# Performance work log

Hardware: AMD Instinct MI355X
Metric: run time of the kernel (lower is better)

Reference implementation:

```python
import jax, jax.numpy as jnp
import numpy as np

B, D_IN = 2048, 16
Q, QD = 512, 2
H = 128

def setup_inputs() -> dict:
    key = jax.random.key(0)
    ks = jax.random.split(key, 7)
    return {
        "input": jax.random.normal(ks[0], (B, D_IN), dtype=jnp.float32),
        "eq_param": jax.random.normal(ks[1], (QD, 1), dtype=jnp.float32),
        "quad_x": jax.random.uniform(ks[2], (Q, QD), dtype=jnp.float32),
        "W1": jax.random.normal(ks[3], (QD + D_IN, H), dtype=jnp.float32) * (1.0 / np.sqrt(QD + D_IN)),
        "b1": jnp.zeros((H,), dtype=jnp.float32),
        "W2": jax.random.normal(ks[4], (H, 1), dtype=jnp.float32) * (1.0 / np.sqrt(H)),
        "b2": jnp.zeros((1,), dtype=jnp.float32),
    }

def reference(input, eq_param, quad_x, W1, b1, W2, b2):
    # input: [B, d_in], quad_x: [Q, qd]
    b, d = input.shape
    q, qd = quad_x.shape
    # x = quad_x.repeat(B,1) -> [B,Q,qd]; z = input repeated per quad row -> [B,Q,d]
    x = jnp.broadcast_to(quad_x[None, :, :], (b, q, qd))
    z = jnp.broadcast_to(input[:, None, :], (b, q, d))
    concat = jnp.concatenate([x, z], axis=-1)            # [B,Q,qd+d]
    h = jnp.tanh(concat @ W1 + b1)                       # [B,Q,H]
    lhs = h @ W2 + b2                                    # [B,Q,1]  (mlp_x)
    y = jnp.sin(x @ eq_param)                            # [B,Q,1]  (r_func)
    rhs = lhs * y
    # per-row segment sum over Q quadrature points (and scalar out dim)
    out = jnp.sum(rhs, axis=(1, 2))[:, None]             # [B,1]
    return out
```

## Files before the change

### kernel.cpp

```cpp
#include <hip/hip_runtime.h>
#include <math.h>

#define B_N   2048
#define D_IN_ 16
#define Q_N   512
#define H_N   128

#define QCHUNK 32
#define QPC    (QCHUNK / 4)
#define NQC_A  8
#define QCHUNK_B 16
#define QPC_B    (QCHUNK_B / 4)
#define NQC_B    16

#define NB     8
#define RPB    16
#define NRB    (B_N / RPB)

static constexpr float kC = 2.88539008177792681472f;

__global__ __launch_bounds__(256, 4) void fused_kernel_a(
    const float* __restrict__ input,
    const float* __restrict__ eq,
    const float* __restrict__ qx,
    const float* __restrict__ W1,
    const float* __restrict__ b1,
    const float* __restrict__ W2,
    const float* __restrict__ b2,
    float* __restrict__ out)
{
    __shared__ float c_s[QPC * 8 * H_N];
    __shared__ float in_s[RPB * D_IN_];
    __shared__ float qx_s[QCHUNK * 2];
    __shared__ float y_s[QCHUNK];
    __shared__ float part[4][NB];
    __shared__ float Sc_s, w2sum_s;

    const int t    = threadIdx.x;
    const int rb   = blockIdx.x & (NRB - 1);
    const int qc   = blockIdx.x >> 7;
    const int h    = t & 127;
    const int bg   = t >> 7;
    const int lane = t & 63;
    const int w    = t >> 6;

    in_s[t] = input[rb * (RPB * D_IN_) + t];
    if (t < QCHUNK * 2) qx_s[t] = qx[qc * (QCHUNK * 2) + t];
    if (w == 0) {
        float s = 0.0f;
        if (lane < QCHUNK) {
            const int q = qc * QCHUNK + lane;
            const float a  = fmaf(qx[2 * q + 1], eq[1], qx[2 * q] * eq[0]);
            const float yv = sinf(a);
            y_s[lane] = -2.0f * yv;
            s = yv;
        }
        #pragma unroll
        for (int off = 32; off >= 1; off >>= 1)
            s += __shfl_down(s, off, 64);
        if (lane == 0) Sc_s = s;
    }
    if (w == 1) {
        float s = W2[lane] + W2[64 + lane];
        #pragma unroll
        for (int off = 32; off >= 1; off >>= 1)
            s += __shfl_down(s, off, 64);
        if (lane == 0) w2sum_s = s;
    }
    const float w2 = W2[h];
    __syncthreads();

    {
        const float w1a = W1[h], w1b = W1[H_N + h], bh = b1[h];
        #pragma unroll
        for (int k = 0; k < 4; ++k) {
            const int qd = bg * 4 + k;
            float n0 = 0, n1 = 0, n2 = 0, n3 = 0;
            float p1 = 0, p2 = 0, p3 = 0, p4 = 0;
            #pragma unroll
            for (int i = 0; i < 4; ++i) {
                const int ql = qd * 4 + i;
                const float x0 = qx_s[2 * ql], x1 = qx_s[2 * ql + 1];
                const float u = fmaf(x1, w1b, fmaf(x0, w1a, bh));
                const float E = __builtin_amdgcn_exp2f(u * kC);
                const float y = y_s[ql];
                n3 = fmaf(E, n2, fmaf(y, p3, n3));
                n2 = fmaf(E, n1, fmaf(y, p2, n2));
                n1 = fmaf(E, n0, fmaf(y, p1, n1));
                n0 = n0 + y;
                p4 = fmaf(E, p3, p4);
                p3 = fmaf(E, p2, p3);
                p2 = fmaf(E, p1, p2);
                p1 = p1 + E;
            }
            float* dst = c_s + qd * (8 * H_N) + h;
            dst[0 * H_N] = n0; dst[1 * H_N] = n1;
            dst[2 * H_N] = n2; dst[3 * H_N] = n3;
            dst[4 * H_N] = p1; dst[5 * H_N] = p2;
            dst[6 * H_N] = p3; dst[7 * H_N] = p4;
        }
    }

    float F[NB], acc[NB];
    {
        float s[NB];
        #pragma unroll
        for (int r = 0; r < NB; ++r) s[r] = 0.0f;
        const float4* in4 = (const float4*)in_s;
        #pragma unroll
        for (int k = 0; k < 4; ++k) {
            const float wa = W1[(2 + 4 * k + 0) * H_N + h];
            const float wb = W1[(2 + 4 * k + 1) * H_N + h];
            const float wc = W1[(2 + 4 * k + 2) * H_N + h];
            const float wd = W1[(2 + 4 * k + 3) * H_N + h];
            #pragma unroll
            for (int r = 0; r < NB; ++r) {
                const float4 a = in4[(bg * NB + r) * 4 + k];
                float sr = s[r];
                sr = fmaf(a.x, wa, sr);
                sr = fmaf(a.y, wb, sr);
                sr = fmaf(a.z, wc, sr);
                sr = fmaf(a.w, wd, sr);
                s[r] = sr;
            }
        }
        #pragma unroll
        for (int r = 0; r < NB; ++r) {
            F[r] = __builtin_amdgcn_exp2f(s[r] * kC);
            acc[r] = 0.0f;
        }
    }
    __syncthreads();

    #pragma unroll 2
    for (int qd = 0; qd < QPC; ++qd) {
        const float* cp = c_s + qd * (8 * H_N) + h;
        const float n0 = cp[0 * H_N], n1 = cp[1 * H_N];
        const float n2 = cp[2 * H_N], n3 = cp[3 * H_N];
        const float c1 = cp[4 * H_N], c2 = cp[5 * H_N];
        const float c3 = cp[6 * H_N], c4 = cp[7 * H_N];
        #pragma unroll
        for (int r = 0; r < NB; ++r) {
            const float Fr  = F[r];
            const float den = fmaf(fmaf(fmaf(fmaf(c4, Fr, c3), Fr, c2), Fr, c1), Fr, 1.0f);
            const float num = fmaf(fmaf(fmaf(n3, Fr, n2), Fr, n1), Fr, n0);
            acc[r] = fmaf(num, __builtin_amdgcn_rcpf(den), acc[r]);
        }
    }

    #pragma unroll
    for (int r = 0; r < NB; ++r) {
        float p = acc[r] * w2;
        #pragma unroll
        for (int off = 32; off >= 1; off >>= 1)
            p += __shfl_down(p, off, 64);
        if (lane == 0) part[w][r] = p;
    }
    __syncthreads();

    if (t < 16) {
        const int r = t & 7, g = t >> 3;
        const float k0c = Sc_s * (w2sum_s + b2[0]);
        const float s = part[2 * g][r] + part[2 * g + 1][r] + k0c;
        atomicAdd(out + rb * RPB + g * NB + r, s);
    }
}

__global__ __launch_bounds__(256, 8) void fused_kernel_b(
    const float* __restrict__ input,
    const float* __restrict__ eq,
    const float* __restrict__ qx,
    const float* __restrict__ W1,
    const float* __restrict__ b1,
    const float* __restrict__ W2,
    const float* __restrict__ b2,
    float* __restrict__ out)
{
    __shared__ float c_s[QPC_B * 8 * H_N];
    __shared__ float in_s[RPB * D_IN_];
    __shared__ float qx_s[QCHUNK_B * 2];
    __shared__ float y_s[QCHUNK_B];
    __shared__ float part[4][NB];
    __shared__ float Sc_s, w2sum_s;

    const int t    = threadIdx.x;
    const int rb   = blockIdx.x & (NRB - 1);
    const int qc   = 16 + (blockIdx.x >> 7);
    const int h    = t & 127;
    const int bg   = t >> 7;
    const int lane = t & 63;
    const int w    = t >> 6;

    in_s[t] = input[rb * (RPB * D_IN_) + t];
    if (t < QCHUNK_B * 2) qx_s[t] = qx[qc * (QCHUNK_B * 2) + t];
    if (w == 0) {
        float s = 0.0f;
        if (lane < QCHUNK_B) {
            const int q = qc * QCHUNK_B + lane;
            const float a  = fmaf(qx[2 * q + 1], eq[1], qx[2 * q] * eq[0]);
            const float yv = sinf(a);
            y_s[lane] = -2.0f * yv;
            s = yv;
        }
        #pragma unroll
        for (int off = 32; off >= 1; off >>= 1)
            s += __shfl_down(s, off, 64);
        if (lane == 0) Sc_s = s;
    }
    if (w == 1) {
        float s = W2[lane] + W2[64 + lane];
        #pragma unroll
        for (int off = 32; off >= 1; off >>= 1)
            s += __shfl_down(s, off, 64);
        if (lane == 0) w2sum_s = s;
    }
    const float w2 = W2[h];
    __syncthreads();

    {
        const float w1a = W1[h], w1b = W1[H_N + h], bh = b1[h];
        #pragma unroll
        for (int k = 0; k < 2; ++k) {
            const int qd = bg * 2 + k;
            float n0 = 0, n1 = 0, n2 = 0, n3 = 0;
            float p1 = 0, p2 = 0, p3 = 0, p4 = 0;
            #pragma unroll
            for (int i = 0; i < 4; ++i) {
                const int ql = qd * 4 + i;
                const float x0 = qx_s[2 * ql], x1 = qx_s[2 * ql + 1];
                const float u = fmaf(x1, w1b, fmaf(x0, w1a, bh));
                const float E = __builtin_amdgcn_exp2f(u * kC);
                const float y = y_s[ql];
                n3 = fmaf(E, n2, fmaf(y, p3, n3));
                n2 = fmaf(E, n1, fmaf(y, p2, n2));
                n1 = fmaf(E, n0, fmaf(y, p1, n1));
                n0 = n0 + y;
                p4 = fmaf(E, p3, p4);
                p3 = fmaf(E, p2, p3);
                p2 = fmaf(E, p1, p2);
                p1 = p1 + E;
            }
            float* dst = c_s + qd * (8 * H_N) + h;
            dst[0 * H_N] = n0; dst[1 * H_N] = n1;
            dst[2 * H_N] = n2; dst[3 * H_N] = n3;
            dst[4 * H_N] = p1; dst[5 * H_N] = p2;
            dst[6 * H_N] = p3; dst[7 * H_N] = p4;
        }
    }

    float F[NB], acc[NB];
    {
        float s[NB];
        #pragma unroll
        for (int r = 0; r < NB; ++r) s[r] = 0.0f;
        const float4* in4 = (const float4*)in_s;
        #pragma unroll
        for (int k = 0; k < 4; ++k) {
            const float wa = W1[(2 + 4 * k + 0) * H_N + h];
            const float wb = W1[(2 + 4 * k + 1) * H_N + h];
            const float wc = W1[(2 + 4 * k + 2) * H_N + h];
            const float wd = W1[(2 + 4 * k + 3) * H_N + h];
            #pragma unroll
            for (int r = 0; r < NB; ++r) {
                const float4 a = in4[(bg * NB + r) * 4 + k];
                float sr = s[r];
                sr = fmaf(a.x, wa, sr);
                sr = fmaf(a.y, wb, sr);
                sr = fmaf(a.z, wc, sr);
                sr = fmaf(a.w, wd, sr);
                s[r] = sr;
            }
        }
        #pragma unroll
        for (int r = 0; r < NB; ++r) {
            F[r] = __builtin_amdgcn_exp2f(s[r] * kC);
            acc[r] = 0.0f;
        }
    }
    __syncthreads();

    #pragma unroll 2
    for (int qd = 0; qd < QPC_B; ++qd) {
        const float* cp = c_s + qd * (8 * H_N) + h;
        const float n0 = cp[0 * H_N], n1 = cp[1 * H_N];
        const float n2 = cp[2 * H_N], n3 = cp[3 * H_N];
        const float c1 = cp[4 * H_N], c2 = cp[5 * H_N];
        const float c3 = cp[6 * H_N], c4 = cp[7 * H_N];
        #pragma unroll
        for (int r = 0; r < NB; ++r) {
            const float Fr  = F[r];
            const float den = fmaf(fmaf(fmaf(fmaf(c4, Fr, c3), Fr, c2), Fr, c1), Fr, 1.0f);
            const float num = fmaf(fmaf(fmaf(n3, Fr, n2), Fr, n1), Fr, n0);
            acc[r] = fmaf(num, __builtin_amdgcn_rcpf(den), acc[r]);
        }
    }

    #pragma unroll
    for (int r = 0; r < NB; ++r) {
        float p = acc[r] * w2;
        #pragma unroll
        for (int off = 32; off >= 1; off >>= 1)
            p += __shfl_down(p, off, 64);
        if (lane == 0) part[w][r] = p;
    }
    __syncthreads();

    if (t < 16) {
        const int r = t & 7, g = t >> 3;
        const float k0c = Sc_s * (w2sum_s + b2[0]);
        const float s = part[2 * g][r] + part[2 * g + 1][r] + k0c;
        atomicAdd(out + rb * RPB + g * NB + r, s);
    }
}

extern "C" void kernel_launch(void* const* d_in, const int* in_sizes, int n_in,
                              void* d_out, int out_size, void* d_ws, size_t ws_size,
                              hipStream_t stream)
{
    (void)in_sizes; (void)n_in; (void)d_ws; (void)ws_size;
    const float* input = (const float*)d_in[0];
    const float* eq    = (const float*)d_in[1];
    const float* qx    = (const float*)d_in[2];
    const float* W1    = (const float*)d_in[3];
    const float* b1    = (const float*)d_in[4];
    const float* W2    = (const float*)d_in[5];
    const float* b2    = (const float*)d_in[6];
    float* out = (float*)d_out;

    hipMemsetAsync(d_out, 0, (size_t)out_size * sizeof(float), stream);
    fused_kernel_a<<<dim3(NRB * NQC_A), dim3(256), 0, stream>>>(
        input, eq, qx, W1, b1, W2, b2, out);
    fused_kernel_b<<<dim3(NRB * NQC_B), dim3(256), 0, stream>>>(
        input, eq, qx, W1, b1, W2, b2, out);
}
```

Before: 87.16 us.

## Split into precompute kernel for F and per-chunk coefficients plus lean main kernel

Adds a precompute kernel that computes the per-row exp factors F (B×H) and the per-quadrature-chunk rational coefficients once and writes them to the workspace. A second kernel then reads them as float4s from global memory and does only the rational evaluation and reduction. This removes the 128-fold redundant coefficient computation and 16-fold redundant F computation done in every block. In exchange it adds an extra launch and about 1 MB of global traffic for F. A fallback fused kernel with swizzled float4 shared storage is kept for when no workspace is provided.

```diff
diff --git a/kernel.cpp b/kernel.cpp
--- a/kernel.cpp
+++ b/kernel.cpp
@@ -7,19 +7,165 @@
 #define H_N   128
 
 #define QCHUNK 32
+#define NQC    (Q_N / QCHUNK)
 #define QPC    (QCHUNK / 4)
-#define NQC_A  8
-#define QCHUNK_B 16
-#define QPC_B    (QCHUNK_B / 4)
-#define NQC_B    16
-
 #define NB     8
 #define RPB    16
 #define NRB    (B_N / RPB)
 
 static constexpr float kC = 2.88539008177792681472f;
 
-__global__ __launch_bounds__(256, 4) void fused_kernel_a(
+#define F_OFF   0
+#define C4_OFF  (B_N * H_N)
+#define SC_OFF  (C4_OFF + NQC * QPC * 2 * H_N * 4)
+#define W2S_OFF (SC_OFF + NQC)
+#define WS_FLOATS (W2S_OFF + 1)
+
+__global__ __launch_bounds__(256, 4) void precompute_kernel(
+    const float* __restrict__ input,
+    const float* __restrict__ eq,
+    const float* __restrict__ qx,
+    const float* __restrict__ W1,
+    const float* __restrict__ b1,
+    const float* __restrict__ W2,
+    float* __restrict__ ws)
+{
+    const int t = threadIdx.x;
+    const int blk = blockIdx.x;
+
+    if (blk < 1024) {
+        const int row = blk * 2 + (t >> 7);
+        const int h   = t & 127;
+        const float* inr = input + row * D_IN_;
+        float s = 0.0f;
+        #pragma unroll
+        for (int d = 0; d < D_IN_; ++d)
+            s = fmaf(inr[d], W1[(2 + d) * H_N + h], s);
+        ws[F_OFF + row * H_N + h] = __builtin_amdgcn_exp2f(s * kC);
+        return;
+    }
+
+    const int qc   = blk - 1024;
+    const int h    = t & 127;
+    const int bg   = t >> 7;
+    const int lane = t & 63;
+    const int w    = t >> 6;
+
+    __shared__ float y_s[QCHUNK];
+
+    if (w == 0) {
+        float s = 0.0f;
+        if (lane < QCHUNK) {
+            const int q = qc * QCHUNK + lane;
+            const float a  = fmaf(qx[2 * q + 1], eq[1], qx[2 * q] * eq[0]);
+            const float yv = sinf(a);
+            y_s[lane] = -2.0f * yv;
+            s = yv;
+        }
+        #pragma unroll
+        for (int off = 32; off >= 1; off >>= 1)
+            s += __shfl_down(s, off, 64);
+        if (lane == 0) ws[SC_OFF + qc] = s;
+    }
+    if (w == 1 && qc == 0) {
+        float s = W2[lane] + W2[64 + lane];
+        #pragma unroll
+        for (int off = 32; off >= 1; off >>= 1)
+            s += __shfl_down(s, off, 64);
+        if (lane == 0) ws[W2S_OFF] = s;
+    }
+    __syncthreads();
+
+    const float w1a = W1[h], w1b = W1[H_N + h], bh = b1[h];
+    float4* c4 = (float4*)(ws + C4_OFF);
+    #pragma unroll
+    for (int k = 0; k < 4; ++k) {
+        const int qd = bg * 4 + k;
+        float n0 = 0, n1 = 0, n2 = 0, n3 = 0;
+        float p1 = 0, p2 = 0, p3 = 0, p4 = 0;
+        #pragma unroll
+        for (int i = 0; i < 4; ++i) {
+            const int ql = qd * 4 + i;
+            const float x0 = qx[qc * (QCHUNK * 2) + 2 * ql];
+            const float x1 = qx[qc * (QCHUNK * 2) + 2 * ql + 1];
+            const float u = fmaf(x1, w1b, fmaf(x0, w1a, bh));
+            const float E = __builtin_amdgcn_exp2f(u * kC);
+            const float y = y_s[ql];
+            n3 = fmaf(E, n2, fmaf(y, p3, n3));
+            n2 = fmaf(E, n1, fmaf(y, p2, n2));
+            n1 = fmaf(E, n0, fmaf(y, p1, n1));
+            n0 = n0 + y;
+            p4 = fmaf(E, p3, p4);
+            p3 = fmaf(E, p2, p3);
+            p2 = fmaf(E, p1, p2);
+            p1 = p1 + E;
+        }
+        const int base = (qc * QPC + qd) * 2;
+        c4[(base + 0) * H_N + h] = make_float4(n0, n1, n2, n3);
+        c4[(base + 1) * H_N + h] = make_float4(p1, p2, p3, p4);
+    }
+}
+
+__global__ __launch_bounds__(256, 4) void main_kernel(
+    const float* __restrict__ ws,
+    const float* __restrict__ W2,
+    const float* __restrict__ b2,
+    float* __restrict__ out)
+{
+    __shared__ float part[4][NB];
+
+    const int t    = threadIdx.x;
+    const int rb   = blockIdx.x & (NRB - 1);
+    const int qc   = blockIdx.x >> 7;
+    const int h    = t & 127;
+    const int bg   = t >> 7;
+    const int lane = t & 63;
+    const int w    = t >> 6;
+
+    const float w2 = W2[h];
+
+    float F[NB], acc[NB];
+    #pragma unroll
+    for (int r = 0; r < NB; ++r) {
+        const int row = rb * RPB + bg * NB + r;
+        F[r]   = ws[F_OFF + row * H_N + h];
+        acc[r] = 0.0f;
+    }
+
+    const float4* c4 = (const float4*)(ws + C4_OFF);
+    #pragma unroll 2
+    for (int qd = 0; qd < QPC; ++qd) {
+        const int base = (qc * QPC + qd) * 2;
+        const float4 cn = c4[(base + 0) * H_N + h];
+        const float4 cp = c4[(base + 1) * H_N + h];
+        #pragma unroll
+        for (int r = 0; r < NB; ++r) {
+            const float Fr  = F[r];
+            const float den = fmaf(fmaf(fmaf(fmaf(cp.w, Fr, cp.z), Fr, cp.y), Fr, cp.x), Fr, 1.0f);
+            const float num = fmaf(fmaf(fmaf(cn.w, Fr, cn.z), Fr, cn.y), Fr, cn.x);
+            acc[r] = fmaf(num, __builtin_amdgcn_rcpf(den), acc[r]);
+        }
+    }
+
+    #pragma unroll
+    for (int r = 0; r < NB; ++r) {
+        float p = acc[r] * w2;
+        #pragma unroll
+        for (int off = 32; off >= 1; off >>= 1)
+            p += __shfl_down(p, off, 64);
+        if (lane == 0) part[w][r] = p;
+    }
+    __syncthreads();
+
+    if (t < 16) {
+        const int r = t & 7, g = t >> 3;
+        const float k0c = ws[SC_OFF + qc] * (ws[W2S_OFF] + b2[0]);
+        const float s = part[2 * g][r] + part[2 * g + 1][r] + k0c;
+        atomicAdd(out + rb * RPB + g * NB + r, s);
+    }
+}
+
+__global__ __launch_bounds__(256, 4) void fused_fallback(
     const float* __restrict__ input,
     const float* __restrict__ eq,
     const float* __restrict__ qx,
@@ -29,7 +175,7 @@
     const float* __restrict__ b2,
     float* __restrict__ out)
 {
-    __shared__ float c_s[QPC * 8 * H_N];
+    __shared__ float4 c4_s[QPC * 256];
     __shared__ float in_s[RPB * D_IN_];
     __shared__ float qx_s[QCHUNK * 2];
     __shared__ float y_s[QCHUNK];
@@ -43,6 +189,8 @@
     const int bg   = t >> 7;
     const int lane = t & 63;
     const int w    = t >> 6;
+    const int cwn = (2 * h)     ^ (((2 * h)     >> 3) & 7);
+    const int cwp = (2 * h + 1) ^ (((2 * h + 1) >> 3) & 7);
 
     in_s[t] = input[rb * (RPB * D_IN_) + t];
     if (t < QCHUNK * 2) qx_s[t] = qx[qc * (QCHUNK * 2) + t];
@@ -93,11 +241,9 @@
                 p2 = fmaf(E, p1, p2);
                 p1 = p1 + E;
             }
-            float* dst = c_s + qd * (8 * H_N) + h;
-            dst[0 * H_N] = n0; dst[1 * H_N] = n1;
-            dst[2 * H_N] = n2; dst[3 * H_N] = n3;
-            dst[4 * H_N] = p1; dst[5 * H_N] = p2;
-            dst[6 * H_N] = p3; dst[7 * H_N] = p4;
+            float4* dst = c4_s + qd * 256;
+            dst[cwn] = make_float4(n0, n1, n2, n3);
+            dst[cwp] = make_float4(p1, p2, p3, p4);
         }
     }
 
@@ -134,16 +280,13 @@
 
     #pragma unroll 2
     for (int qd = 0; qd < QPC; ++qd) {
-        const float* cp = c_s + qd * (8 * H_N) + h;
-        const float n0 = cp[0 * H_N], n1 = cp[1 * H_N];
-        const float n2 = cp[2 * H_N], n3 = cp[3 * H_N];
-        const float c1 = cp[4 * H_N], c2 = cp[5 * H_N];
-        const float c3 = cp[6 * H_N], c4 = cp[7 * H_N];
+        const float4 cn = c4_s[qd * 256 + cwn];
+        const float4 cp = c4_s[qd * 256 + cwp];
         #pragma unroll
         for (int r = 0; r < NB; ++r) {
             const float Fr  = F[r];
-            const float den = fmaf(fmaf(fmaf(fmaf(c4, Fr, c3), Fr, c2), Fr, c1), Fr, 1.0f);
-            const float num = fmaf(fmaf(fmaf(n3, Fr, n2), Fr, n1), Fr, n0);
+            const float den = fmaf(fmaf(fmaf(fmaf(cp.w, Fr, cp.z), Fr, cp.y), Fr, cp.x), Fr, 1.0f);
+            const float num = fmaf(fmaf(fmaf(cn.w, Fr, cn.z), Fr, cn.y), Fr, cn.x);
             acc[r] = fmaf(num, __builtin_amdgcn_rcpf(den), acc[r]);
         }
     }
@@ -166,158 +309,11 @@
     }
 }
 
-__global__ __launch_bounds__(256, 8) void fused_kernel_b(
-    const float* __restrict__ input,
-    const float* __restrict__ eq,
-    const float* __restrict__ qx,
-    const float* __restrict__ W1,
-    const float* __restrict__ b1,
-    const float* __restrict__ W2,
-    const float* __restrict__ b2,
-    float* __restrict__ out)
-{
-    __shared__ float c_s[QPC_B * 8 * H_N];
-    __shared__ float in_s[RPB * D_IN_];
-    __shared__ float qx_s[QCHUNK_B * 2];
-    __shared__ float y_s[QCHUNK_B];
-    __shared__ float part[4][NB];
-    __shared__ float Sc_s, w2sum_s;
-
-    const int t    = threadIdx.x;
-    const int rb   = blockIdx.x & (NRB - 1);
-    const int qc   = 16 + (blockIdx.x >> 7);
-    const int h    = t & 127;
-    const int bg   = t >> 7;
-    const int lane = t & 63;
-    const int w    = t >> 6;
-
-    in_s[t] = input[rb * (RPB * D_IN_) + t];
-    if (t < QCHUNK_B * 2) qx_s[t] = qx[qc * (QCHUNK_B * 2) + t];
-    if (w == 0) {
-        float s = 0.0f;
-        if (lane < QCHUNK_B) {
-            const int q = qc * QCHUNK_B + lane;
-            const float a  = fmaf(qx[2 * q + 1], eq[1], qx[2 * q] * eq[0]);
-            const float yv = sinf(a);
-            y_s[lane] = -2.0f * yv;
-            s = yv;
-        }
-        #pragma unroll
-        for (int off = 32; off >= 1; off >>= 1)
-            s += __shfl_down(s, off, 64);
-        if (lane == 0) Sc_s = s;
-    }
-    if (w == 1) {
-        float s = W2[lane] + W2[64 + lane];
-        #pragma unroll
-        for (int off = 32; off >= 1; off >>= 1)
-            s += __shfl_down(s, off, 64);
-        if (lane == 0) w2sum_s = s;
-    }
-    const float w2 = W2[h];
-    __syncthreads();
-
-    {
-        const float w1a = W1[h], w1b = W1[H_N + h], bh = b1[h];
-        #pragma unroll
-        for (int k = 0; k < 2; ++k) {
-            const int qd = bg * 2 + k;
-            float n0 = 0, n1 = 0, n2 = 0, n3 = 0;
-            float p1 = 0, p2 = 0, p3 = 0, p4 = 0;
-            #pragma unroll
-            for (int i = 0; i < 4; ++i) {
-                const int ql = qd * 4 + i;
-                const float x0 = qx_s[2 * ql], x1 = qx_s[2 * ql + 1];
-                const float u = fmaf(x1, w1b, fmaf(x0, w1a, bh));
-                const float E = __builtin_amdgcn_exp2f(u * kC);
-                const float y = y_s[ql];
-                n3 = fmaf(E, n2, fmaf(y, p3, n3));
-                n2 = fmaf(E, n1, fmaf(y, p2, n2));
-                n1 = fmaf(E, n0, fmaf(y, p1, n1));
-                n0 = n0 + y;
-                p4 = fmaf(E, p3, p4);
-                p3 = fmaf(E, p2, p3);
-                p2 = fmaf(E, p1, p2);
-                p1 = p1 + E;
-            }
-            float* dst = c_s + qd * (8 * H_N) + h;
-            dst[0 * H_N] = n0; dst[1 * H_N] = n1;
-            dst[2 * H_N] = n2; dst[3 * H_N] = n3;
-            dst[4 * H_N] = p1; dst[5 * H_N] = p2;
-            dst[6 * H_N] = p3; dst[7 * H_N] = p4;
-        }
-    }
-
-    float F[NB], acc[NB];
-    {
-        float s[NB];
-        #pragma unroll
-        for (int r = 0; r < NB; ++r) s[r] = 0.0f;
-        const float4* in4 = (const float4*)in_s;
-        #pragma unroll
-        for (int k = 0; k < 4; ++k) {
-            const float wa = W1[(2 + 4 * k + 0) * H_N + h];
-            const float wb = W1[(2 + 4 * k + 1) * H_N + h];
-            const float wc = W1[(2 + 4 * k + 2) * H_N + h];
-            const float wd = W1[(2 + 4 * k + 3) * H_N + h];
-            #pragma unroll
-            for (int r = 0; r < NB; ++r) {
-                const float4 a = in4[(bg * NB + r) * 4 + k];
-                float sr = s[r];
-                sr = fmaf(a.x, wa, sr);
-                sr = fmaf(a.y, wb, sr);
-                sr = fmaf(a.z, wc, sr);
-                sr = fmaf(a.w, wd, sr);
-                s[r] = sr;
-            }
-        }
-        #pragma unroll
-        for (int r = 0; r < NB; ++r) {
-            F[r] = __builtin_amdgcn_exp2f(s[r] * kC);
-            acc[r] = 0.0f;
-        }
-    }
-    __syncthreads();
-
-    #pragma unroll 2
-    for (int qd = 0; qd < QPC_B; ++qd) {
-        const float* cp = c_s + qd * (8 * H_N) + h;
-        const float n0 = cp[0 * H_N], n1 = cp[1 * H_N];
-        const float n2 = cp[2 * H_N], n3 = cp[3 * H_N];
-        const float c1 = cp[4 * H_N], c2 = cp[5 * H_N];
-        const float c3 = cp[6 * H_N], c4 = cp[7 * H_N];
-        #pragma unroll
-        for (int r = 0; r < NB; ++r) {
-            const float Fr  = F[r];
-            const float den = fmaf(fmaf(fmaf(fmaf(c4, Fr, c3), Fr, c2), Fr, c1), Fr, 1.0f);
-            const float num = fmaf(fmaf(fmaf(n3, Fr, n2), Fr, n1), Fr, n0);
-            acc[r] = fmaf(num, __builtin_amdgcn_rcpf(den), acc[r]);
-        }
-    }
-
-    #pragma unroll
-    for (int r = 0; r < NB; ++r) {
-        float p = acc[r] * w2;
-        #pragma unroll
-        for (int off = 32; off >= 1; off >>= 1)
-            p += __shfl_down(p, off, 64);
-        if (lane == 0) part[w][r] = p;
-    }
-    __syncthreads();
-
-    if (t < 16) {
-        const int r = t & 7, g = t >> 3;
-        const float k0c = Sc_s * (w2sum_s + b2[0]);
-        const float s = part[2 * g][r] + part[2 * g + 1][r] + k0c;
-        atomicAdd(out + rb * RPB + g * NB + r, s);
-    }
-}
-
 extern "C" void kernel_launch(void* const* d_in, const int* in_sizes, int n_in,
                               void* d_out, int out_size, void* d_ws, size_t ws_size,
                               hipStream_t stream)
 {
-    (void)in_sizes; (void)n_in; (void)d_ws; (void)ws_size;
+    (void)in_sizes; (void)n_in;
     const float* input = (const float*)d_in[0];
     const float* eq    = (const float*)d_in[1];
     const float* qx    = (const float*)d_in[2];
@@ -328,8 +324,15 @@
     float* out = (float*)d_out;
 
     hipMemsetAsync(d_out, 0, (size_t)out_size * sizeof(float), stream);
-    fused_kernel_a<<<dim3(NRB * NQC_A), dim3(256), 0, stream>>>(
-        input, eq, qx, W1, b1, W2, b2, out);
-    fused_kernel_b<<<dim3(NRB * NQC_B), dim3(256), 0, stream>>>(
-        input, eq, qx, W1, b1, W2, b2, out);
+
+    if (d_ws != nullptr && ws_size >= (size_t)WS_FLOATS * sizeof(float)) {
+        float* ws = (float*)d_ws;
+        precompute_kernel<<<dim3(1024 + NQC), dim3(256), 0, stream>>>(
+            input, eq, qx, W1, b1, W2, ws);
+        main_kernel<<<dim3(NRB * NQC), dim3(256), 0, stream>>>(
+            ws, W2, b2, out);
+    } else {
+        fused_fallback<<<dim3(NRB * NQC), dim3(256), 0, stream>>>(
+            input, eq, qx, W1, b1, W2, b2, out);
+    }
 }
```

New measurement: 80.69 us. 7.4% less time.
